# Optimization experiments

Hardware: AMD Instinct MI355X
Metric: run time of the kernel (lower is better)

Reference implementation:

```python
import jax, jax.numpy as jnp
import numpy as np


def setup_inputs() -> dict:
    key = jax.random.key(0)
    k1, k2 = jax.random.split(key)
    B, N, M, D = 8, 8192, 8192, 3
    input1 = jax.random.normal(k1, (B, N, D), dtype=jnp.float32)
    input2 = jax.random.normal(k2, (B, M, D), dtype=jnp.float32)
    return {"input1": input1, "input2": input2}


def reference(input1, input2):
    # input1: [B, N, 3], input2: [B, M, 3]
    # Squared pairwise distances via ||x||^2 + ||y||^2 - 2<x,y>
    sq1 = jnp.sum(input1 * input1, axis=-1)          # [B, N]
    sq2 = jnp.sum(input2 * input2, axis=-1)          # [B, M]
    inner = jnp.einsum('bnd,bmd->bnm', input1, input2)  # [B, N, M]
    d = sq1[:, :, None] + sq2[:, None, :] - 2.0 * inner  # [B, N, M]
    d = jnp.maximum(d, 0.0)  # numerical guard
    dist1 = jnp.min(d, axis=2)  # [B, N] NN in input2 for each point of input1
    dist2 = jnp.min(d, axis=1)  # [B, M] NN in input1 for each point of input2
    loss = jnp.mean(dist1) + jnp.mean(dist2)
    return loss
```

## Files before the change

### kernel.cpp

```cpp
#include <hip/hip_runtime.h>


typedef _Float16 half8 __attribute__((ext_vector_type(8)));
typedef float    f16x  __attribute__((ext_vector_type(16)));

constexpr int B       = 8;
constexpr int NPTS    = 8192;
constexpr int TOTAL   = B * NPTS;
constexpr int NSTRIP  = 256;
constexpr int NSTRIPS = NPTS / NSTRIP;
constexpr int MH      = 4;
constexpr int MHALF   = NPTS / MH;
constexpr int CHUNK   = 512;
constexpr int NCHUNK  = MHALF / CHUNK;
constexpr int NWAVE   = 8;

__device__ __forceinline__ float colmin16(const f16x& a)
{
    float m0 = fminf(fminf(a[0],  a[1]),  a[2]);
    float m1 = fminf(fminf(a[3],  a[4]),  a[5]);
    float m2 = fminf(fminf(a[6],  a[7]),  a[8]);
    float m3 = fminf(fminf(a[9],  a[10]), a[11]);
    float m4 = fminf(fminf(a[12], a[13]), a[14]);
    return fminf(fminf(fminf(m0, m1), m2), fminf(fminf(m3, m4), a[15]));
}

__global__ __launch_bounds__(512, 8) void chamfer_mfma(
    const float* __restrict__ in1, const float* __restrict__ in2,
    float* __restrict__ d1p, float* __restrict__ d2p, float* __restrict__ out)
{
    const int b     = blockIdx.z;
    const int strip = blockIdx.x;
    const int mh    = blockIdx.y;
    const int wave  = threadIdx.x >> 6;
    const int lane  = threadIdx.x & 63;
    const int col   = lane & 31;
    const int half  = lane >> 5;

    if ((blockIdx.x | blockIdx.y | blockIdx.z) == 0 && threadIdx.x == 0)
        *out = 0.0f;

    __shared__ _Float16 ldsB[CHUNK * 16];
    __shared__ float    d2w[NWAVE][CHUNK];

    const int nbase = strip * NSTRIP + wave * 32;
    half8 afrag;
    {
        const float* a = in1 + ((size_t)b * NPTS + nbase + col) * 3;
        float x = a[0], y = a[1], z = a[2];
        float sq = fmaf(x, x, fmaf(y, y, z * z));
        _Float16 xh = (_Float16)x, yh = (_Float16)y, zh = (_Float16)z;
        _Float16 xl = (_Float16)(x - (float)xh);
        _Float16 yl = (_Float16)(y - (float)yh);
        _Float16 zl = (_Float16)(z - (float)zh);
        _Float16 sh = (_Float16)sq, sl = (_Float16)(sq - (float)sh);
        half8 lo = {xh, yh, zh, xl, yl, zl, xh, yh};
        half8 hi = {zh, sh, sl, (_Float16)1.f, (_Float16)1.f,
                    (_Float16)0.f, (_Float16)0.f, (_Float16)0.f};
        afrag = half ? hi : lo;
    }

    f16x MN1, zacc;
#pragma unroll
    for (int r = 0; r < 16; ++r) { MN1[r] = 1e30f; zacc[r] = 0.0f; }

    const float* Craw = in2 + ((size_t)b * NPTS + mh * MHALF) * 3;
    float* d2 = d2p + ((size_t)b * NSTRIPS + strip) * NPTS + mh * MHALF;

    float px, py, pz;
    {
        const float* cp = Craw + (size_t)threadIdx.x * 3;
        px = cp[0]; py = cp[1]; pz = cp[2];
    }

    for (int c = 0; c < NCHUNK; ++c) {
        half8 plo, phi;
        {
            float x = -2.f * px, y = -2.f * py, z = -2.f * pz;
            float sq = fmaf(px, px, fmaf(py, py, pz * pz));
            _Float16 xh = (_Float16)x, yh = (_Float16)y, zh = (_Float16)z;
            _Float16 xl = (_Float16)(x - (float)xh);
            _Float16 yl = (_Float16)(y - (float)yh);
            _Float16 zl = (_Float16)(z - (float)zh);
            _Float16 sh = (_Float16)sq, sl = (_Float16)(sq - (float)sh);
            plo = half8{xh, yh, zh, xh, yh, zh, xl, yl};
            phi = half8{zl, (_Float16)1.f, (_Float16)1.f, sh, sl,
                        (_Float16)0.f, (_Float16)0.f, (_Float16)0.f};
        }
        __syncthreads();
        *(half8*)&ldsB[(threadIdx.x >> 5) * 512 + (threadIdx.x & 31) * 8]       = plo;
        *(half8*)&ldsB[(threadIdx.x >> 5) * 512 + 256 + (threadIdx.x & 31) * 8] = phi;
        if (c > 0) {
            float v = d2w[0][threadIdx.x];
#pragma unroll
            for (int w = 1; w < NWAVE; ++w) v = fminf(v, d2w[w][threadIdx.x]);
            d2[(c - 1) * CHUNK + threadIdx.x] = fmaxf(v, 0.0f);
        }
        if (c + 1 < NCHUNK) {
            const float* cp = Craw + (size_t)((c + 1) * CHUNK + threadIdx.x) * 3;
            px = cp[0]; py = cp[1]; pz = cp[2];
        }
        __syncthreads();

#pragma unroll 2
        for (int t = 0; t < CHUNK / 32; t += 2) {
            half8 bfA = *(const half8*)&ldsB[ t      * 512 + lane * 8];
            half8 bfB = *(const half8*)&ldsB[(t + 1) * 512 + lane * 8];
            f16x accA = __builtin_amdgcn_mfma_f32_32x32x16_f16(afrag, bfA, zacc, 0, 0, 0);
            f16x accB = __builtin_amdgcn_mfma_f32_32x32x16_f16(afrag, bfB, zacc, 0, 0, 0);

#pragma unroll
            for (int r = 0; r < 16; ++r)
                MN1[r] = fminf(fminf(accA[r], accB[r]), MN1[r]);

            float vA = colmin16(accA);
            float vB = colmin16(accB);
            vA = fminf(vA, __shfl_xor(vA, 32, 64));
            vB = fminf(vB, __shfl_xor(vB, 32, 64));
            d2w[wave][(t + half) * 32 + col] = half ? vB : vA;
        }
    }
    __syncthreads();
    {
        float v = d2w[0][threadIdx.x];
#pragma unroll
        for (int w = 1; w < NWAVE; ++w) v = fminf(v, d2w[w][threadIdx.x]);
        d2[(NCHUNK - 1) * CHUNK + threadIdx.x] = fmaxf(v, 0.0f);
    }

#pragma unroll
    for (int m = 1; m <= 16; m <<= 1)
#pragma unroll
        for (int r = 0; r < 16; ++r)
            MN1[r] = fminf(MN1[r], __shfl_xor(MN1[r], m, 64));
    if (col == 0) {
        float* d1 = d1p + ((size_t)b * MH + mh) * NPTS + nbase;
#pragma unroll
        for (int r = 0; r < 16; ++r)
            d1[(r & 3) + 8 * (r >> 2) + 4 * half] = MN1[r];
    }
}

__global__ __launch_bounds__(64) void reduce_kernel(
    const float* __restrict__ d1p, const float* __restrict__ d2p,
    float* __restrict__ out)
{
    int g  = blockIdx.x * 64 + threadIdx.x;
    int b  = g >> 11;
    int mq = g & 2047;

    const float4* p2 = (const float4*)(d2p + (size_t)b * NSTRIPS * NPTS) + mq;
    float4 v2 = p2[0];
#pragma unroll 8
    for (int s = 1; s < NSTRIPS; ++s) {
        float4 t = p2[(size_t)s * (NPTS / 4)];
        v2.x = fminf(v2.x, t.x); v2.y = fminf(v2.y, t.y);
        v2.z = fminf(v2.z, t.z); v2.w = fminf(v2.w, t.w);
    }
    const float4* p1 = (const float4*)(d1p + (size_t)b * MH * NPTS) + mq;
    float4 a = p1[0];
#pragma unroll
    for (int s = 1; s < MH; ++s) {
        float4 t = p1[(size_t)s * (NPTS / 4)];
        a.x = fminf(a.x, t.x); a.y = fminf(a.y, t.y);
        a.z = fminf(a.z, t.z); a.w = fminf(a.w, t.w);
    }
    float v = fmaxf(a.x, 0.0f) + fmaxf(a.y, 0.0f)
            + fmaxf(a.z, 0.0f) + fmaxf(a.w, 0.0f)
            + v2.x + v2.y + v2.z + v2.w;

#pragma unroll
    for (int off = 32; off; off >>= 1)
        v += __shfl_down(v, off, 64);
    if (threadIdx.x == 0)
        atomicAdd(out, v * (1.0f / (float)TOTAL));
}

extern "C" void kernel_launch(void* const* d_in, const int* in_sizes, int n_in,
                              void* d_out, int out_size, void* d_ws, size_t ws_size,
                              hipStream_t stream)
{
    const float* in1 = (const float*)d_in[0];
    const float* in2 = (const float*)d_in[1];
    float* out = (float*)d_out;

    char* ws = (char*)d_ws;
    float* d1p = (float*)ws;
    float* d2p = (float*)(ws + (size_t)MH * TOTAL * 4);

    chamfer_mfma<<<dim3(NSTRIPS, MH, B), 512, 0, stream>>>(
        in1, in2, d1p, d2p, out);
    reduce_kernel<<<TOTAL / 4 / 64, 64, 0, stream>>>(d1p, d2p, out);
}
```

Baseline: 100.9 us.

## Compute both NN directions as separate row-min passes instead of column reductions

```diff
diff --git a/kernel.cpp b/kernel.cpp
--- a/kernel.cpp
+++ b/kernel.cpp
@@ -13,40 +13,47 @@
 constexpr int MHALF   = NPTS / MH;
 constexpr int CHUNK   = 512;
 constexpr int NCHUNK  = MHALF / CHUNK;
-constexpr int NWAVE   = 8;
 
-__device__ __forceinline__ float colmin16(const f16x& a)
+__device__ __forceinline__ void packB(float cx, float cy, float cz,
+                                      half8& plo, half8& phi)
 {
-    float m0 = fminf(fminf(a[0],  a[1]),  a[2]);
-    float m1 = fminf(fminf(a[3],  a[4]),  a[5]);
-    float m2 = fminf(fminf(a[6],  a[7]),  a[8]);
-    float m3 = fminf(fminf(a[9],  a[10]), a[11]);
-    float m4 = fminf(fminf(a[12], a[13]), a[14]);
-    return fminf(fminf(fminf(m0, m1), m2), fminf(fminf(m3, m4), a[15]));
+    float x = -2.f * cx, y = -2.f * cy, z = -2.f * cz;
+    float sq = fmaf(cx, cx, fmaf(cy, cy, cz * cz));
+    _Float16 xh = (_Float16)x, yh = (_Float16)y, zh = (_Float16)z;
+    _Float16 xl = (_Float16)(x - (float)xh);
+    _Float16 yl = (_Float16)(y - (float)yh);
+    _Float16 zl = (_Float16)(z - (float)zh);
+    _Float16 sh = (_Float16)sq, sl = (_Float16)(sq - (float)sh);
+    plo = half8{xh, yh, zh, xh, yh, zh, xl, yl};
+    phi = half8{zl, (_Float16)1.f, (_Float16)1.f, sh, sl,
+                (_Float16)0.f, (_Float16)0.f, (_Float16)0.f};
 }
 
-__global__ __launch_bounds__(512, 8) void chamfer_mfma(
+__global__ __launch_bounds__(512, 8) void nn_mfma(
     const float* __restrict__ in1, const float* __restrict__ in2,
-    float* __restrict__ d1p, float* __restrict__ d2p, float* __restrict__ out)
+    float* __restrict__ minp, float* __restrict__ out)
 {
     const int b     = blockIdx.z;
     const int strip = blockIdx.x;
-    const int mh    = blockIdx.y;
+    const int pass  = blockIdx.y / MH;
+    const int mh    = blockIdx.y % MH;
     const int wave  = threadIdx.x >> 6;
     const int lane  = threadIdx.x & 63;
     const int col   = lane & 31;
     const int half  = lane >> 5;
 
+    const float* Apts = pass ? in2 : in1;
+    const float* Bpts = pass ? in1 : in2;
+
     if ((blockIdx.x | blockIdx.y | blockIdx.z) == 0 && threadIdx.x == 0)
         *out = 0.0f;
 
     __shared__ _Float16 ldsB[CHUNK * 16];
-    __shared__ float    d2w[NWAVE][CHUNK];
 
     const int nbase = strip * NSTRIP + wave * 32;
     half8 afrag;
     {
-        const float* a = in1 + ((size_t)b * NPTS + nbase + col) * 3;
+        const float* a = Apts + ((size_t)b * NPTS + nbase + col) * 3;
         float x = a[0], y = a[1], z = a[2];
         float sq = fmaf(x, x, fmaf(y, y, z * z));
         _Float16 xh = (_Float16)x, yh = (_Float16)y, zh = (_Float16)z;
@@ -64,8 +71,7 @@
 #pragma unroll
     for (int r = 0; r < 16; ++r) { MN1[r] = 1e30f; zacc[r] = 0.0f; }
 
-    const float* Craw = in2 + ((size_t)b * NPTS + mh * MHALF) * 3;
-    float* d2 = d2p + ((size_t)b * NSTRIPS + strip) * NPTS + mh * MHALF;
+    const float* Craw = Bpts + ((size_t)b * NPTS + mh * MHALF) * 3;
 
     float px, py, pz;
     {
@@ -75,34 +81,17 @@
 
     for (int c = 0; c < NCHUNK; ++c) {
         half8 plo, phi;
-        {
-            float x = -2.f * px, y = -2.f * py, z = -2.f * pz;
-            float sq = fmaf(px, px, fmaf(py, py, pz * pz));
-            _Float16 xh = (_Float16)x, yh = (_Float16)y, zh = (_Float16)z;
-            _Float16 xl = (_Float16)(x - (float)xh);
-            _Float16 yl = (_Float16)(y - (float)yh);
-            _Float16 zl = (_Float16)(z - (float)zh);
-            _Float16 sh = (_Float16)sq, sl = (_Float16)(sq - (float)sh);
-            plo = half8{xh, yh, zh, xh, yh, zh, xl, yl};
-            phi = half8{zl, (_Float16)1.f, (_Float16)1.f, sh, sl,
-                        (_Float16)0.f, (_Float16)0.f, (_Float16)0.f};
-        }
+        packB(px, py, pz, plo, phi);
         __syncthreads();
         *(half8*)&ldsB[(threadIdx.x >> 5) * 512 + (threadIdx.x & 31) * 8]       = plo;
         *(half8*)&ldsB[(threadIdx.x >> 5) * 512 + 256 + (threadIdx.x & 31) * 8] = phi;
-        if (c > 0) {
-            float v = d2w[0][threadIdx.x];
-#pragma unroll
-            for (int w = 1; w < NWAVE; ++w) v = fminf(v, d2w[w][threadIdx.x]);
-            d2[(c - 1) * CHUNK + threadIdx.x] = fmaxf(v, 0.0f);
-        }
         if (c + 1 < NCHUNK) {
             const float* cp = Craw + (size_t)((c + 1) * CHUNK + threadIdx.x) * 3;
             px = cp[0]; py = cp[1]; pz = cp[2];
         }
         __syncthreads();
 
-#pragma unroll 2
+#pragma unroll
         for (int t = 0; t < CHUNK / 32; t += 2) {
             half8 bfA = *(const half8*)&ldsB[ t      * 512 + lane * 8];
             half8 bfB = *(const half8*)&ldsB[(t + 1) * 512 + lane * 8];
@@ -112,20 +101,7 @@
 #pragma unroll
             for (int r = 0; r < 16; ++r)
                 MN1[r] = fminf(fminf(accA[r], accB[r]), MN1[r]);
-
-            float vA = colmin16(accA);
-            float vB = colmin16(accB);
-            vA = fminf(vA, __shfl_xor(vA, 32, 64));
-            vB = fminf(vB, __shfl_xor(vB, 32, 64));
-            d2w[wave][(t + half) * 32 + col] = half ? vB : vA;
         }
-    }
-    __syncthreads();
-    {
-        float v = d2w[0][threadIdx.x];
-#pragma unroll
-        for (int w = 1; w < NWAVE; ++w) v = fminf(v, d2w[w][threadIdx.x]);
-        d2[(NCHUNK - 1) * CHUNK + threadIdx.x] = fmaxf(v, 0.0f);
     }
 
 #pragma unroll
@@ -134,40 +110,35 @@
         for (int r = 0; r < 16; ++r)
             MN1[r] = fminf(MN1[r], __shfl_xor(MN1[r], m, 64));
     if (col == 0) {
-        float* d1 = d1p + ((size_t)b * MH + mh) * NPTS + nbase;
+        float* o = minp + (((size_t)pass * B + b) * MH + mh) * NPTS + nbase;
 #pragma unroll
         for (int r = 0; r < 16; ++r)
-            d1[(r & 3) + 8 * (r >> 2) + 4 * half] = MN1[r];
+            o[(r & 3) + 8 * (r >> 2) + 4 * half] = MN1[r];
     }
 }
 
 __global__ __launch_bounds__(64) void reduce_kernel(
-    const float* __restrict__ d1p, const float* __restrict__ d2p,
-    float* __restrict__ out)
+    const float* __restrict__ minp, float* __restrict__ out)
 {
     int g  = blockIdx.x * 64 + threadIdx.x;
     int b  = g >> 11;
     int mq = g & 2047;
 
-    const float4* p2 = (const float4*)(d2p + (size_t)b * NSTRIPS * NPTS) + mq;
-    float4 v2 = p2[0];
-#pragma unroll 8
-    for (int s = 1; s < NSTRIPS; ++s) {
-        float4 t = p2[(size_t)s * (NPTS / 4)];
-        v2.x = fminf(v2.x, t.x); v2.y = fminf(v2.y, t.y);
-        v2.z = fminf(v2.z, t.z); v2.w = fminf(v2.w, t.w);
+    float v = 0.0f;
+#pragma unroll
+    for (int p = 0; p < 2; ++p) {
+        const float4* pp =
+            (const float4*)(minp + (((size_t)p * B + b) * MH) * NPTS) + mq;
+        float4 a = pp[0];
+#pragma unroll
+        for (int s = 1; s < MH; ++s) {
+            float4 t = pp[(size_t)s * (NPTS / 4)];
+            a.x = fminf(a.x, t.x); a.y = fminf(a.y, t.y);
+            a.z = fminf(a.z, t.z); a.w = fminf(a.w, t.w);
+        }
+        v += fmaxf(a.x, 0.0f) + fmaxf(a.y, 0.0f)
+           + fmaxf(a.z, 0.0f) + fmaxf(a.w, 0.0f);
     }
-    const float4* p1 = (const float4*)(d1p + (size_t)b * MH * NPTS) + mq;
-    float4 a = p1[0];
-#pragma unroll
-    for (int s = 1; s < MH; ++s) {
-        float4 t = p1[(size_t)s * (NPTS / 4)];
-        a.x = fminf(a.x, t.x); a.y = fminf(a.y, t.y);
-        a.z = fminf(a.z, t.z); a.w = fminf(a.w, t.w);
-    }
-    float v = fmaxf(a.x, 0.0f) + fmaxf(a.y, 0.0f)
-            + fmaxf(a.z, 0.0f) + fmaxf(a.w, 0.0f)
-            + v2.x + v2.y + v2.z + v2.w;
 
 #pragma unroll
     for (int off = 32; off; off >>= 1)
@@ -184,11 +155,9 @@
     const float* in2 = (const float*)d_in[1];
     float* out = (float*)d_out;
 
-    char* ws = (char*)d_ws;
-    float* d1p = (float*)ws;
-    float* d2p = (float*)(ws + (size_t)MH * TOTAL * 4);
+    float* minp = (float*)d_ws;
 
-    chamfer_mfma<<<dim3(NSTRIPS, MH, B), 512, 0, stream>>>(
-        in1, in2, d1p, d2p, out);
-    reduce_kernel<<<TOTAL / 4 / 64, 64, 0, stream>>>(d1p, d2p, out);
+    nn_mfma<<<dim3(NSTRIPS, 2 * MH, B), 512, 0, stream>>>(
+        in1, in2, minp, out);
+    reduce_kernel<<<TOTAL / 4 / 64, 64, 0, stream>>>(minp, out);
 }
```

Measured after the change: 105.1 us. 1.04x slower.
